# Performance work log

Measured on AMD Instinct MI355X. Metric: run time of the kernel, lower is better.

Reference implementation:

```python
import jax, jax.numpy as jnp
import numpy as np

T, B, D_IN, R, D_OUT = 256, 64, 512, 2048, 128
SPARSITY, BETA, THRESH = 0.8, 0.9, 1.0


def setup_inputs() -> dict:
    key = jax.random.key(0)
    ks = jax.random.split(key, 6)
    lim_rec = float(np.sqrt(3.0 / R))  # VarianceScaling(1.0,'fan_avg','uniform') with fan_in=fan_out=R
    return {
        "x_seq": jax.random.normal(ks[0], (T, B, D_IN), jnp.float32),
        "w_in": jax.random.normal(ks[1], (D_IN, R), jnp.float32) / np.sqrt(D_IN).astype(np.float32),
        "b_in": jnp.zeros((R,), jnp.float32),
        "w_rec": jax.random.uniform(ks[2], (R, R), jnp.float32, -lim_rec, lim_rec),
        "w_head": jax.random.normal(ks[3], (R, D_OUT), jnp.float32) / np.sqrt(R).astype(np.float32),
        "b_head": jnp.zeros((D_OUT,), jnp.float32),
    }


def reference(x_seq, w_in, b_in, w_rec, w_head, b_head):
    n = R * R
    keep = max(1, int(n * (1.0 - SPARSITY)))
    scores = jnp.abs(w_rec).reshape(-1)
    thresh = jnp.sort(scores)[n - keep]  # k-th largest of |w_rec| (same threshold as top_k)
    mask = (jnp.abs(w_rec) >= thresh).astype(w_rec.dtype)
    w_eff = w_rec * mask

    # input projection is time-parallel; hoist it out of the scan
    drive_in = jnp.einsum('tbd,dr->tbr', x_seq, w_in) + b_in  # [T,B,R]

    def step(carry, drive_t):
        V, prev_s = carry
        cur = drive_t + prev_s @ w_eff          # sparse recurrent drive
        V = BETA * V + cur                      # LIF integrate (leak + input)
        s = (V > THRESH).astype(x_seq.dtype)    # heaviside spike
        V = V - s * THRESH                      # soft reset
        logits = s @ w_head + b_head
        return (V, s), (logits, jnp.mean(s))

    init = (jnp.zeros((B, R), x_seq.dtype), jnp.zeros((B, R), x_seq.dtype))
    _, (logits_seq, sr_seq) = jax.lax.scan(step, init, drive_in)

    readout = jnp.mean(logits_seq, axis=0)  # readout mode 'mean'
    spike_rate = jnp.asarray([jnp.mean(sr_seq)])
    active_ratio = jnp.mean(mask)
    return readout, logits_seq, spike_rate, active_ratio
```

## Files before the change

kernel.cpp:

```cpp
#include <hip/hip_runtime.h>
#include <hip/hip_bf16.h>
#include <stdint.h>

#define TT 256
#define BB 64
#define DIN 512
#define RR 2048
#define DOUT 128
#define NTOT (RR*RR)
#define NKEEP 838860
#define BETA 0.9f
#define VTH 1.0f


__global__ void k_init(uint32_t* __restrict__ p, int n) {
    int i = blockIdx.x * blockDim.x + threadIdx.x;
    int stride = gridDim.x * blockDim.x;
    for (; i < n; i += stride) p[i] = 0u;
}

__global__ void k_hist(const float* __restrict__ w_rec, uint32_t* __restrict__ hist,
                       const uint32_t* __restrict__ state, int p) {
    __shared__ uint32_t lh[256];
    lh[threadIdx.x] = 0u;
    __syncthreads();
    uint32_t prefix = (p > 0) ? state[0] : 0u;
    int sh = 24 - 8 * p;
    int i = blockIdx.x * 256 + threadIdx.x;
    int stride = gridDim.x * 256;
    for (; i < NTOT; i += stride) {
        uint32_t u = __float_as_uint(fabsf(w_rec[i]));
        bool ok = (p == 0) || ((u >> (sh + 8)) == prefix);
        if (ok) atomicAdd(&lh[(u >> sh) & 255u], 1u);
    }
    __syncthreads();
    uint32_t v = lh[threadIdx.x];
    if (v) atomicAdd(&hist[threadIdx.x], v);
}

__global__ void k_select(uint32_t* __restrict__ hist, uint32_t* __restrict__ state, int p) {
    __shared__ uint32_t lh[256];
    int tid = threadIdx.x;
    lh[tid] = hist[tid];
    hist[tid] = 0u;
    __syncthreads();
    if (tid == 0) {
        uint32_t remaining = (p == 0) ? (uint32_t)NKEEP : state[1];
        int bin = 255;
        for (; bin > 0; --bin) {
            uint32_t c = lh[bin];
            if (c >= remaining) break;
            remaining -= c;
        }
        uint32_t pref = (p == 0) ? 0u : state[0];
        pref = (pref << 8) | (uint32_t)bin;
        state[0] = pref;
        state[1] = remaining;
        if (p == 3) state[2] = pref;
    }
}

__global__ void k_maskcount(float* __restrict__ w, const uint32_t* __restrict__ state,
                            uint32_t* __restrict__ cnts) {
    uint32_t th = state[2];
    uint32_t c = 0;
    int i = blockIdx.x * blockDim.x + threadIdx.x;
    int stride = gridDim.x * blockDim.x;
    for (; i < NTOT / 4; i += stride) {
        float4 v = *(float4*)&w[i * 4];
        if ((__float_as_uint(v.x) & 0x7fffffffu) >= th) c++; else v.x = 0.0f;
        if ((__float_as_uint(v.y) & 0x7fffffffu) >= th) c++; else v.y = 0.0f;
        if ((__float_as_uint(v.z) & 0x7fffffffu) >= th) c++; else v.z = 0.0f;
        if ((__float_as_uint(v.w) & 0x7fffffffu) >= th) c++; else v.w = 0.0f;
        *(float4*)&w[i * 4] = v;
    }
    for (int off = 32; off > 0; off >>= 1) c += __shfl_down(c, off);
    if ((threadIdx.x & 63) == 0 && c) atomicAdd(&cnts[1], c);
}

__global__ __launch_bounds__(256) void k_drive(const float* __restrict__ x,
                                               const float* __restrict__ w_in,
                                               const float* __restrict__ b_in,
                                               float* __restrict__ drive) {
    __shared__ float As[8][128];
    __shared__ float Bs[8][128];
    const int m0 = blockIdx.x * 128;
    const int n0 = blockIdx.y * 128;
    const int tid = threadIdx.x;
    const int tx = tid & 15, ty = tid >> 4;
    const int ar = tid >> 1;
    const int ak = (tid & 1) * 4;
    const int bk = tid >> 5;
    const int bc = (tid & 31) * 4;
    float acc[8][8];
    #pragma unroll
    for (int i = 0; i < 8; ++i)
        #pragma unroll
        for (int j = 0; j < 8; ++j) acc[i][j] = 0.0f;

    for (int k0 = 0; k0 < DIN; k0 += 8) {
        float4 av = *(const float4*)&x[(m0 + ar) * DIN + k0 + ak];
        float4 bv = *(const float4*)&w_in[(size_t)(k0 + bk) * RR + n0 + bc];
        __syncthreads();
        As[ak + 0][ar] = av.x; As[ak + 1][ar] = av.y;
        As[ak + 2][ar] = av.z; As[ak + 3][ar] = av.w;
        *(float4*)&Bs[bk][bc] = bv;
        __syncthreads();
        #pragma unroll
        for (int kk = 0; kk < 8; ++kk) {
            float a[8], b[8];
            *(float4*)&a[0] = *(const float4*)&As[kk][ty * 8];
            *(float4*)&a[4] = *(const float4*)&As[kk][ty * 8 + 4];
            *(float4*)&b[0] = *(const float4*)&Bs[kk][tx * 8];
            *(float4*)&b[4] = *(const float4*)&Bs[kk][tx * 8 + 4];
            #pragma unroll
            for (int i = 0; i < 8; ++i)
                #pragma unroll
                for (int j = 0; j < 8; ++j)
                    acc[i][j] = fmaf(a[i], b[j], acc[i][j]);
        }
    }
    float bb[8];
    #pragma unroll
    for (int j = 0; j < 8; ++j) bb[j] = b_in[n0 + tx * 8 + j];
    #pragma unroll
    for (int i = 0; i < 8; ++i) {
        size_t row = (size_t)(m0 + ty * 8 + i) * RR + n0 + tx * 8;
        float4 v0, v1;
        v0.x = acc[i][0] + bb[0]; v0.y = acc[i][1] + bb[1];
        v0.z = acc[i][2] + bb[2]; v0.w = acc[i][3] + bb[3];
        v1.x = acc[i][4] + bb[4]; v1.y = acc[i][5] + bb[5];
        v1.z = acc[i][6] + bb[6]; v1.w = acc[i][7] + bb[7];
        *(float4*)&drive[row] = v0;
        *(float4*)&drive[row + 4] = v1;
    }
}

__global__ __launch_bounds__(256) void k_scan(const float* __restrict__ w_rec,
                                              const float* __restrict__ drive,
                                              uint32_t* mask, unsigned long long* flags,
                                              uint32_t* cnts) {
    __shared__ __align__(16) int s_list[RR];
    __shared__ int s_n;
    __shared__ uint32_t s_red[4];

    const int tid = threadIdx.x;
    const int blk = blockIdx.x;
    const int cg = blk & 7;
    const int b = blk >> 3;
    const int col = (cg << 8) + tid;
    const int w = tid >> 6;
    const int lane = tid & 63;
    const char* Wp = (const char*)(w_rec + col);

    float V = 0.f;
    uint32_t scnt = 0;
    float dv = drive[(size_t)b * RR + col];

    for (int t = 0; t < TT; ++t) {
        float a = dv;
        if (t > 0) {
            if (tid == 0) {
                const unsigned long long* fl = &flags[(size_t)(t - 1) * BB + b];
                while (__hip_atomic_load(fl, __ATOMIC_RELAXED, __HIP_MEMORY_SCOPE_AGENT)
                       != ~0ull)
                    __builtin_amdgcn_s_sleep(1);
            }
            __syncthreads();
            if (tid < 64) {
                uint32_t m = __hip_atomic_load(&mask[((size_t)(t - 1) * BB + b) * 64 + tid],
                                               __ATOMIC_RELAXED, __HIP_MEMORY_SCOPE_AGENT);
                int p = __popc(m);
                int off = p;
                #pragma unroll
                for (int d = 1; d < 64; d <<= 1) {
                    int o = __shfl_up(off, d);
                    if (tid >= d) off += o;
                }
                if (tid == 63) s_n = off;
                int e = off - p;
                int base = tid << 5;
                while (m) {
                    int bit = __builtin_ctz(m);
                    m &= m - 1;
                    s_list[e++] = (base + bit) << 13;
                }
            }
            __syncthreads();
            const int n = s_n;
            int i = 0;
            for (; i + 16 <= n; i += 16) {
                int4 o0 = *(const int4*)&s_list[i];
                int4 o1 = *(const int4*)&s_list[i + 4];
                int4 o2 = *(const int4*)&s_list[i + 8];
                int4 o3 = *(const int4*)&s_list[i + 12];
                float v[16];
                v[0]  = *(const float*)(Wp + o0.x);
                v[1]  = *(const float*)(Wp + o0.y);
                v[2]  = *(const float*)(Wp + o0.z);
                v[3]  = *(const float*)(Wp + o0.w);
                v[4]  = *(const float*)(Wp + o1.x);
                v[5]  = *(const float*)(Wp + o1.y);
                v[6]  = *(const float*)(Wp + o1.z);
                v[7]  = *(const float*)(Wp + o1.w);
                v[8]  = *(const float*)(Wp + o2.x);
                v[9]  = *(const float*)(Wp + o2.y);
                v[10] = *(const float*)(Wp + o2.z);
                v[11] = *(const float*)(Wp + o2.w);
                v[12] = *(const float*)(Wp + o3.x);
                v[13] = *(const float*)(Wp + o3.y);
                v[14] = *(const float*)(Wp + o3.z);
                v[15] = *(const float*)(Wp + o3.w);
                #pragma unroll
                for (int j = 0; j < 16; ++j) a += v[j];
            }
            for (; i + 4 <= n; i += 4) {
                int4 o = *(const int4*)&s_list[i];
                float v0 = *(const float*)(Wp + o.x);
                float v1 = *(const float*)(Wp + o.y);
                float v2 = *(const float*)(Wp + o.z);
                float v3 = *(const float*)(Wp + o.w);
                a += v0; a += v1; a += v2; a += v3;
            }
            for (; i < n; ++i) a += *(const float*)(Wp + s_list[i]);
        }

        V = BETA * V + a;
        bool sp = V > VTH;
        if (sp) V -= VTH;

        if (t + 1 < TT)
            dv = drive[((size_t)(t + 1) * BB + b) * RR + col];

        unsigned long long bal = __ballot(sp);
        if (lane == 0) {
            __hip_atomic_store(
                (unsigned long long*)&mask[((size_t)t * BB + b) * 64] + (cg * 4 + w),
                bal, __ATOMIC_RELAXED, __HIP_MEMORY_SCOPE_AGENT);
            scnt += (uint32_t)__popcll(bal);
        }
        __syncthreads();
        if (tid == 0)
            __hip_atomic_store((uint8_t*)&flags[(size_t)t * BB + b] + cg, (uint8_t)0xFF,
                               __ATOMIC_RELEASE, __HIP_MEMORY_SCOPE_AGENT);
    }

    if (lane == 0) s_red[w] = scnt;
    __syncthreads();
    if (tid == 0) {
        uint32_t s = s_red[0] + s_red[1] + s_red[2] + s_red[3];
        if (s) atomicAdd(&cnts[0], s);
    }
}

__global__ __launch_bounds__(128) void k_head(const uint32_t* __restrict__ mask,
                                              const float* __restrict__ w_head,
                                              const float* __restrict__ b_head,
                                              float* __restrict__ logits) {
    __shared__ uint32_t sm[64];
    int tb = blockIdx.x;
    int tid = threadIdx.x;
    if (tid < 64) sm[tid] = mask[tb * 64 + tid];
    __syncthreads();
    float acc = b_head[tid];
    for (int w = 0; w < 64; ++w) {
        uint32_t m = sm[w];
        int base = w << 5;
        while (m) {
            int bit = __builtin_ctz(m);
            m &= m - 1;
            acc += w_head[(size_t)(base + bit) * DOUT + tid];
        }
    }
    logits[(size_t)tb * DOUT + tid] = acc;
}

__global__ __launch_bounds__(128) void k_readout(const float* __restrict__ logits,
                                                 float* __restrict__ readout) {
    int b = blockIdx.x, cidx = threadIdx.x;
    float s = 0.0f;
    for (int t = 0; t < TT; ++t)
        s += logits[(size_t)t * (BB * DOUT) + b * DOUT + cidx];
    readout[b * DOUT + cidx] = s * (1.0f / (float)TT);
}

__global__ void k_scalars(const uint32_t* __restrict__ cnts, float* __restrict__ out) {
    if (threadIdx.x == 0 && blockIdx.x == 0) {
        out[BB * DOUT + TT * BB * DOUT]     = (float)cnts[0] / (float)(TT * BB * RR);
        out[BB * DOUT + TT * BB * DOUT + 1] = (float)cnts[1] / (float)NTOT;
    }
}

extern "C" void kernel_launch(void* const* d_in, const int* in_sizes, int n_in,
                              void* d_out, int out_size, void* d_ws, size_t ws_size,
                              hipStream_t stream) {
    const float* x      = (const float*)d_in[0];
    const float* w_in   = (const float*)d_in[1];
    const float* b_in   = (const float*)d_in[2];
    float*       w_rec  = (float*)d_in[3];
    const float* w_head = (const float*)d_in[4];
    const float* b_head = (const float*)d_in[5];
    float* out = (float*)d_out;

    float*    drive = (float*)d_ws;
    uint32_t* mask  = (uint32_t*)((char*)d_ws + 134217728u);
    unsigned long long* flags = (unsigned long long*)(mask + (TT * BB * 64));
    uint32_t* hist  = (uint32_t*)(flags + TT * BB);
    uint32_t* state = hist + 256;
    uint32_t* cnts  = state + 8;

    k_init<<<64, 256, 0, stream>>>((uint32_t*)flags, TT * BB * 2 + 256 + 8 + 2);

    for (int p = 0; p < 4; ++p) {
        k_hist<<<1024, 256, 0, stream>>>(w_rec, hist, state, p);
        k_select<<<1, 256, 0, stream>>>(hist, state, p);
    }
    k_maskcount<<<1024, 256, 0, stream>>>(w_rec, state, cnts);

    k_drive<<<dim3(128, 16), 256, 0, stream>>>(x, w_in, b_in, drive);

    k_scan<<<512, 256, 0, stream>>>(w_rec, drive, mask, flags, cnts);

    k_head<<<TT * BB, 128, 0, stream>>>(mask, w_head, b_head, out + BB * DOUT);
    k_readout<<<BB, 128, 0, stream>>>(out + BB * DOUT, out);
    k_scalars<<<1, 64, 0, stream>>>(cnts, out);
}
```

Measured before the change: 5.007 ms.

## Swizzle masked recurrent weights and decouple scan wavefronts with per-wave flags

The masking kernel now also XOR-swizzles 64-column groups inside each row of the recurrent weight matrix, so each scan wavefront reads its columns from a row-dependent rotated location. This is meant to spread the gather traffic across memory channels. The scan kernel drops its block-wide barriers. Each wavefront waits on a 32-bit flag, builds its own spike list and publishes its ballot with an atomic fetch-or, which removes intra-block synchronisation from the recurrent loop. The cost is four times the shared-memory lists, more atomics on the flags, and a swizzle kernel launched with 2048 blocks of 1024 threads.

```diff
diff --git a/kernel.cpp b/kernel.cpp
--- a/kernel.cpp
+++ b/kernel.cpp
@@ -60,22 +60,36 @@
     }
 }
 
-__global__ void k_maskcount(float* __restrict__ w, const uint32_t* __restrict__ state,
-                            uint32_t* __restrict__ cnts) {
-    uint32_t th = state[2];
+__global__ __launch_bounds__(1024) void k_swz(float* __restrict__ w,
+                                              const uint32_t* __restrict__ state,
+                                              uint32_t* __restrict__ cnts) {
+    const int r = blockIdx.x;
+    const uint32_t th = state[2];
+    const int m = r & 31;
+    const int tid = threadIdx.x;
     uint32_t c = 0;
-    int i = blockIdx.x * blockDim.x + threadIdx.x;
-    int stride = gridDim.x * blockDim.x;
-    for (; i < NTOT / 4; i += stride) {
-        float4 v = *(float4*)&w[i * 4];
-        if ((__float_as_uint(v.x) & 0x7fffffffu) >= th) c++; else v.x = 0.0f;
-        if ((__float_as_uint(v.y) & 0x7fffffffu) >= th) c++; else v.y = 0.0f;
-        if ((__float_as_uint(v.z) & 0x7fffffffu) >= th) c++; else v.z = 0.0f;
-        if ((__float_as_uint(v.w) & 0x7fffffffu) >= th) c++; else v.w = 0.0f;
-        *(float4*)&w[i * 4] = v;
+    if (m == 0) {
+        for (int k = tid; k < RR; k += 1024) {
+            float v = w[(size_t)r * RR + k];
+            if ((__float_as_uint(v) & 0x7fffffffu) >= th) c++;
+            else w[(size_t)r * RR + k] = 0.0f;
+        }
+    } else {
+        const int h = 31 - __clz(m);
+        const int p = tid >> 6;
+        const int lane = tid & 63;
+        const int g = ((p >> h) << (h + 1)) | (p & ((1 << h) - 1));
+        const int g2 = g ^ m;
+        const size_t i1 = (size_t)r * RR + (g << 6) + lane;
+        const size_t i2 = (size_t)r * RR + (g2 << 6) + lane;
+        float v1 = w[i1], v2 = w[i2];
+        if ((__float_as_uint(v1) & 0x7fffffffu) >= th) c++; else v1 = 0.0f;
+        if ((__float_as_uint(v2) & 0x7fffffffu) >= th) c++; else v2 = 0.0f;
+        w[i1] = v2;
+        w[i2] = v1;
     }
     for (int off = 32; off > 0; off >>= 1) c += __shfl_down(c, off);
-    if ((threadIdx.x & 63) == 0 && c) atomicAdd(&cnts[1], c);
+    if ((tid & 63) == 0 && c) atomicAdd(&cnts[1], c);
 }
 
 __global__ __launch_bounds__(256) void k_drive(const float* __restrict__ x,
@@ -136,22 +150,23 @@
     }
 }
 
-__global__ __launch_bounds__(256) void k_scan(const float* __restrict__ w_rec,
-                                              const float* __restrict__ drive,
-                                              uint32_t* mask, unsigned long long* flags,
-                                              uint32_t* cnts) {
-    __shared__ __align__(16) int s_list[RR];
-    __shared__ int s_n;
-    __shared__ uint32_t s_red[4];
+__global__ __launch_bounds__(256, 2) void k_scan(const float* __restrict__ w_rec,
+                                                 const float* __restrict__ drive,
+                                                 unsigned long long* mask,
+                                                 uint32_t* flags, uint32_t* cnts) {
+    __shared__ __align__(16) int s_list[4 * RR];
 
     const int tid = threadIdx.x;
     const int blk = blockIdx.x;
     const int cg = blk & 7;
     const int b = blk >> 3;
-    const int col = (cg << 8) + tid;
     const int w = tid >> 6;
     const int lane = tid & 63;
-    const char* Wp = (const char*)(w_rec + col);
+    const int g = cg * 4 + w;
+    const int col = (g << 6) + lane;
+    int* wl = &s_list[w << 11];
+    const char* Wp = (const char*)w_rec + (lane << 2);
+    const uint32_t fbit = 1u << g;
 
     float V = 0.f;
     uint32_t scnt = 0;
@@ -160,69 +175,62 @@
     for (int t = 0; t < TT; ++t) {
         float a = dv;
         if (t > 0) {
-            if (tid == 0) {
-                const unsigned long long* fl = &flags[(size_t)(t - 1) * BB + b];
-                while (__hip_atomic_load(fl, __ATOMIC_RELAXED, __HIP_MEMORY_SCOPE_AGENT)
-                       != ~0ull)
-                    __builtin_amdgcn_s_sleep(1);
+            const uint32_t* fl = &flags[(t - 1) * BB + b];
+            while (__hip_atomic_load(fl, __ATOMIC_RELAXED, __HIP_MEMORY_SCOPE_AGENT)
+                   != 0xFFFFFFFFu)
+                __builtin_amdgcn_s_sleep(1);
+            asm volatile("" ::: "memory");
+            uint32_t m = __hip_atomic_load(
+                (const uint32_t*)(mask + (size_t)((t - 1) * BB + b) * 32) + lane,
+                __ATOMIC_RELAXED, __HIP_MEMORY_SCOPE_AGENT);
+            int p = __popc(m);
+            int off = p;
+            #pragma unroll
+            for (int d = 1; d < 64; d <<= 1) {
+                int o = __shfl_up(off, d);
+                if (lane >= d) off += o;
             }
-            __syncthreads();
-            if (tid < 64) {
-                uint32_t m = __hip_atomic_load(&mask[((size_t)(t - 1) * BB + b) * 64 + tid],
-                                               __ATOMIC_RELAXED, __HIP_MEMORY_SCOPE_AGENT);
-                int p = __popc(m);
-                int off = p;
+            const int n = __shfl(off, 63);
+            int e = off - p;
+            int base = lane << 5;
+            while (m) {
+                int bit = __builtin_ctz(m);
+                m &= m - 1;
+                int row = base + bit;
+                wl[e++] = (row << 13) | ((((row & 31) ^ g)) << 8);
+            }
+            __threadfence_block();
+            int i = 0;
+            for (; i + 32 <= n; i += 32) {
+                int4 o[8];
                 #pragma unroll
-                for (int d = 1; d < 64; d <<= 1) {
-                    int o = __shfl_up(off, d);
-                    if (tid >= d) off += o;
+                for (int j = 0; j < 8; ++j) o[j] = *(const int4*)&wl[i + 4 * j];
+                float v[32];
+                #pragma unroll
+                for (int j = 0; j < 8; ++j) {
+                    v[4 * j + 0] = *(const float*)(Wp + o[j].x);
+                    v[4 * j + 1] = *(const float*)(Wp + o[j].y);
+                    v[4 * j + 2] = *(const float*)(Wp + o[j].z);
+                    v[4 * j + 3] = *(const float*)(Wp + o[j].w);
                 }
-                if (tid == 63) s_n = off;
-                int e = off - p;
-                int base = tid << 5;
-                while (m) {
-                    int bit = __builtin_ctz(m);
-                    m &= m - 1;
-                    s_list[e++] = (base + bit) << 13;
-                }
+                #pragma unroll
+                for (int j = 0; j < 32; ++j) a += v[j];
             }
-            __syncthreads();
-            const int n = s_n;
-            int i = 0;
-            for (; i + 16 <= n; i += 16) {
-                int4 o0 = *(const int4*)&s_list[i];
-                int4 o1 = *(const int4*)&s_list[i + 4];
-                int4 o2 = *(const int4*)&s_list[i + 8];
-                int4 o3 = *(const int4*)&s_list[i + 12];
-                float v[16];
-                v[0]  = *(const float*)(Wp + o0.x);
-                v[1]  = *(const float*)(Wp + o0.y);
-                v[2]  = *(const float*)(Wp + o0.z);
-                v[3]  = *(const float*)(Wp + o0.w);
-                v[4]  = *(const float*)(Wp + o1.x);
-                v[5]  = *(const float*)(Wp + o1.y);
-                v[6]  = *(const float*)(Wp + o1.z);
-                v[7]  = *(const float*)(Wp + o1.w);
-                v[8]  = *(const float*)(Wp + o2.x);
-                v[9]  = *(const float*)(Wp + o2.y);
-                v[10] = *(const float*)(Wp + o2.z);
-                v[11] = *(const float*)(Wp + o2.w);
-                v[12] = *(const float*)(Wp + o3.x);
-                v[13] = *(const float*)(Wp + o3.y);
-                v[14] = *(const float*)(Wp + o3.z);
-                v[15] = *(const float*)(Wp + o3.w);
-                #pragma unroll
-                for (int j = 0; j < 16; ++j) a += v[j];
+            for (; i + 8 <= n; i += 8) {
+                int4 o0 = *(const int4*)&wl[i];
+                int4 o1 = *(const int4*)&wl[i + 4];
+                float v0 = *(const float*)(Wp + o0.x);
+                float v1 = *(const float*)(Wp + o0.y);
+                float v2 = *(const float*)(Wp + o0.z);
+                float v3 = *(const float*)(Wp + o0.w);
+                float v4 = *(const float*)(Wp + o1.x);
+                float v5 = *(const float*)(Wp + o1.y);
+                float v6 = *(const float*)(Wp + o1.z);
+                float v7 = *(const float*)(Wp + o1.w);
+                a += v0; a += v1; a += v2; a += v3;
+                a += v4; a += v5; a += v6; a += v7;
             }
-            for (; i + 4 <= n; i += 4) {
-                int4 o = *(const int4*)&s_list[i];
-                float v0 = *(const float*)(Wp + o.x);
-                float v1 = *(const float*)(Wp + o.y);
-                float v2 = *(const float*)(Wp + o.z);
-                float v3 = *(const float*)(Wp + o.w);
-                a += v0; a += v1; a += v2; a += v3;
-            }
-            for (; i < n; ++i) a += *(const float*)(Wp + s_list[i]);
+            for (; i < n; ++i) a += *(const float*)(Wp + wl[i]);
         }
 
         V = BETA * V + a;
@@ -230,27 +238,19 @@
         if (sp) V -= VTH;
 
         if (t + 1 < TT)
-            dv = drive[((size_t)(t + 1) * BB + b) * RR + col];
+            dv = drive[(size_t)(t + 1) * (BB * RR) + (size_t)b * RR + col];
 
         unsigned long long bal = __ballot(sp);
         if (lane == 0) {
-            __hip_atomic_store(
-                (unsigned long long*)&mask[((size_t)t * BB + b) * 64] + (cg * 4 + w),
-                bal, __ATOMIC_RELAXED, __HIP_MEMORY_SCOPE_AGENT);
+            __hip_atomic_store(mask + (size_t)(t * BB + b) * 32 + g, bal,
+                               __ATOMIC_RELAXED, __HIP_MEMORY_SCOPE_AGENT);
             scnt += (uint32_t)__popcll(bal);
-        }
-        __syncthreads();
-        if (tid == 0)
-            __hip_atomic_store((uint8_t*)&flags[(size_t)t * BB + b] + cg, (uint8_t)0xFF,
-                               __ATOMIC_RELEASE, __HIP_MEMORY_SCOPE_AGENT);
-    }
-
-    if (lane == 0) s_red[w] = scnt;
-    __syncthreads();
-    if (tid == 0) {
-        uint32_t s = s_red[0] + s_red[1] + s_red[2] + s_red[3];
-        if (s) atomicAdd(&cnts[0], s);
-    }
+            (void)__hip_atomic_fetch_or(&flags[t * BB + b], fbit,
+                                        __ATOMIC_RELEASE, __HIP_MEMORY_SCOPE_AGENT);
+        }
+    }
+
+    if (lane == 0 && scnt) atomicAdd(&cnts[0], scnt);
 }
 
 __global__ __launch_bounds__(128) void k_head(const uint32_t* __restrict__ mask,
@@ -303,25 +303,26 @@
     float* out = (float*)d_out;
 
     float*    drive = (float*)d_ws;
-    uint32_t* mask  = (uint32_t*)((char*)d_ws + 134217728u);
-    unsigned long long* flags = (unsigned long long*)(mask + (TT * BB * 64));
-    uint32_t* hist  = (uint32_t*)(flags + TT * BB);
+    unsigned long long* mask = (unsigned long long*)((char*)d_ws + 134217728u);
+    uint32_t* flags = (uint32_t*)(mask + (size_t)TT * BB * 32);
+    uint32_t* hist  = flags + TT * BB;
     uint32_t* state = hist + 256;
     uint32_t* cnts  = state + 8;
 
-    k_init<<<64, 256, 0, stream>>>((uint32_t*)flags, TT * BB * 2 + 256 + 8 + 2);
+    k_init<<<64, 256, 0, stream>>>(flags, TT * BB + 256 + 8 + 2);
 
     for (int p = 0; p < 4; ++p) {
         k_hist<<<1024, 256, 0, stream>>>(w_rec, hist, state, p);
         k_select<<<1, 256, 0, stream>>>(hist, state, p);
     }
-    k_maskcount<<<1024, 256, 0, stream>>>(w_rec, state, cnts);
+    k_swz<<<RR, 1024, 0, stream>>>(w_rec, state, cnts);
 
     k_drive<<<dim3(128, 16), 256, 0, stream>>>(x, w_in, b_in, drive);
 
     k_scan<<<512, 256, 0, stream>>>(w_rec, drive, mask, flags, cnts);
 
-    k_head<<<TT * BB, 128, 0, stream>>>(mask, w_head, b_head, out + BB * DOUT);
+    k_head<<<TT * BB, 128, 0, stream>>>((const uint32_t*)mask, w_head, b_head,
+                                        out + BB * DOUT);
     k_readout<<<BB, 128, 0, stream>>>(out + BB * DOUT, out);
     k_scalars<<<1, 64, 0, stream>>>(cnts, out);
 }
```

Measured after the change: 14.84 ms. +196.4%, slower.

## Swizzle recurrent weight columns per row to spread gather accesses across channels

Applied to the files above, without the earlier changes.

Replaces the mask kernel with one that masks w_rec and also XOR-swizzles 64-column groups within each 256-column block based on row index mod 4. The scan's gather addresses apply the matching XOR, so the four wavefronts of a block touch different group offsets for the same spiking row, which should reduce channel/bank aliasing at the 8KB row stride. The gather loop is also unrolled to 32 loads, and the scan gets a launch-bounds occupancy hint. It adds layout complexity and more register pressure.

```diff
diff --git a/kernel.cpp b/kernel.cpp
--- a/kernel.cpp
+++ b/kernel.cpp
@@ -60,22 +60,39 @@
     }
 }
 
-__global__ void k_maskcount(float* __restrict__ w, const uint32_t* __restrict__ state,
-                            uint32_t* __restrict__ cnts) {
-    uint32_t th = state[2];
+__global__ __launch_bounds__(1024) void k_swz(float* __restrict__ w,
+                                              const uint32_t* __restrict__ state,
+                                              uint32_t* __restrict__ cnts) {
+    const int r = blockIdx.x;
+    const uint32_t th = state[2];
+    const int m = r & 3;
+    const int tid = threadIdx.x;
     uint32_t c = 0;
-    int i = blockIdx.x * blockDim.x + threadIdx.x;
-    int stride = gridDim.x * blockDim.x;
-    for (; i < NTOT / 4; i += stride) {
-        float4 v = *(float4*)&w[i * 4];
-        if ((__float_as_uint(v.x) & 0x7fffffffu) >= th) c++; else v.x = 0.0f;
-        if ((__float_as_uint(v.y) & 0x7fffffffu) >= th) c++; else v.y = 0.0f;
-        if ((__float_as_uint(v.z) & 0x7fffffffu) >= th) c++; else v.z = 0.0f;
-        if ((__float_as_uint(v.w) & 0x7fffffffu) >= th) c++; else v.w = 0.0f;
-        *(float4*)&w[i * 4] = v;
+    if (m == 0) {
+        #pragma unroll
+        for (int q = 0; q < 2; ++q) {
+            size_t i = (size_t)r * RR + q * 1024 + tid;
+            float v = w[i];
+            if ((__float_as_uint(v) & 0x7fffffffu) >= th) c++;
+            else w[i] = 0.0f;
+        }
+    } else {
+        const int h = (m == 1) ? 0 : 1;
+        const int chunk = tid >> 7;
+        const int pair = (tid >> 6) & 1;
+        const int lane = tid & 63;
+        const int g  = (h == 0) ? (pair << 1) : pair;
+        const int g2 = g ^ m;
+        const size_t i1 = (size_t)r * RR + chunk * 256 + g  * 64 + lane;
+        const size_t i2 = (size_t)r * RR + chunk * 256 + g2 * 64 + lane;
+        float v1 = w[i1], v2 = w[i2];
+        if ((__float_as_uint(v1) & 0x7fffffffu) >= th) c++; else v1 = 0.0f;
+        if ((__float_as_uint(v2) & 0x7fffffffu) >= th) c++; else v2 = 0.0f;
+        w[i1] = v2;
+        w[i2] = v1;
     }
     for (int off = 32; off > 0; off >>= 1) c += __shfl_down(c, off);
-    if ((threadIdx.x & 63) == 0 && c) atomicAdd(&cnts[1], c);
+    if ((tid & 63) == 0 && c) atomicAdd(&cnts[1], c);
 }
 
 __global__ __launch_bounds__(256) void k_drive(const float* __restrict__ x,
@@ -136,10 +153,10 @@
     }
 }
 
-__global__ __launch_bounds__(256) void k_scan(const float* __restrict__ w_rec,
-                                              const float* __restrict__ drive,
-                                              uint32_t* mask, unsigned long long* flags,
-                                              uint32_t* cnts) {
+__global__ __launch_bounds__(256, 2) void k_scan(const float* __restrict__ w_rec,
+                                                 const float* __restrict__ drive,
+                                                 uint32_t* mask, unsigned long long* flags,
+                                                 uint32_t* cnts) {
     __shared__ __align__(16) int s_list[RR];
     __shared__ int s_n;
     __shared__ uint32_t s_red[4];
@@ -148,10 +165,11 @@
     const int blk = blockIdx.x;
     const int cg = blk & 7;
     const int b = blk >> 3;
-    const int col = (cg << 8) + tid;
     const int w = tid >> 6;
     const int lane = tid & 63;
-    const char* Wp = (const char*)(w_rec + col);
+    const int col = (cg << 8) + tid;
+    const int wx = w << 8;
+    const char* Wq = (const char*)w_rec + (cg << 10) + (lane << 2);
 
     float V = 0.f;
     uint32_t scnt = 0;
@@ -183,46 +201,43 @@
                 while (m) {
                     int bit = __builtin_ctz(m);
                     m &= m - 1;
-                    s_list[e++] = (base + bit) << 13;
+                    int row = base + bit;
+                    s_list[e++] = (row << 13) | ((row & 3) << 8);
                 }
             }
             __syncthreads();
             const int n = s_n;
             int i = 0;
-            for (; i + 16 <= n; i += 16) {
+            for (; i + 32 <= n; i += 32) {
+                int4 o[8];
+                #pragma unroll
+                for (int j = 0; j < 8; ++j) o[j] = *(const int4*)&s_list[i + 4 * j];
+                float v[32];
+                #pragma unroll
+                for (int j = 0; j < 8; ++j) {
+                    v[4 * j + 0] = *(const float*)(Wq + (o[j].x ^ wx));
+                    v[4 * j + 1] = *(const float*)(Wq + (o[j].y ^ wx));
+                    v[4 * j + 2] = *(const float*)(Wq + (o[j].z ^ wx));
+                    v[4 * j + 3] = *(const float*)(Wq + (o[j].w ^ wx));
+                }
+                #pragma unroll
+                for (int j = 0; j < 32; ++j) a += v[j];
+            }
+            for (; i + 8 <= n; i += 8) {
                 int4 o0 = *(const int4*)&s_list[i];
                 int4 o1 = *(const int4*)&s_list[i + 4];
-                int4 o2 = *(const int4*)&s_list[i + 8];
-                int4 o3 = *(const int4*)&s_list[i + 12];
-                float v[16];
-                v[0]  = *(const float*)(Wp + o0.x);
-                v[1]  = *(const float*)(Wp + o0.y);
-                v[2]  = *(const float*)(Wp + o0.z);
-                v[3]  = *(const float*)(Wp + o0.w);
-                v[4]  = *(const float*)(Wp + o1.x);
-                v[5]  = *(const float*)(Wp + o1.y);
-                v[6]  = *(const float*)(Wp + o1.z);
-                v[7]  = *(const float*)(Wp + o1.w);
-                v[8]  = *(const float*)(Wp + o2.x);
-                v[9]  = *(const float*)(Wp + o2.y);
-                v[10] = *(const float*)(Wp + o2.z);
-                v[11] = *(const float*)(Wp + o2.w);
-                v[12] = *(const float*)(Wp + o3.x);
-                v[13] = *(const float*)(Wp + o3.y);
-                v[14] = *(const float*)(Wp + o3.z);
-                v[15] = *(const float*)(Wp + o3.w);
-                #pragma unroll
-                for (int j = 0; j < 16; ++j) a += v[j];
+                float v0 = *(const float*)(Wq + (o0.x ^ wx));
+                float v1 = *(const float*)(Wq + (o0.y ^ wx));
+                float v2 = *(const float*)(Wq + (o0.z ^ wx));
+                float v3 = *(const float*)(Wq + (o0.w ^ wx));
+                float v4 = *(const float*)(Wq + (o1.x ^ wx));
+                float v5 = *(const float*)(Wq + (o1.y ^ wx));
+                float v6 = *(const float*)(Wq + (o1.z ^ wx));
+                float v7 = *(const float*)(Wq + (o1.w ^ wx));
+                a += v0; a += v1; a += v2; a += v3;
+                a += v4; a += v5; a += v6; a += v7;
             }
-            for (; i + 4 <= n; i += 4) {
-                int4 o = *(const int4*)&s_list[i];
-                float v0 = *(const float*)(Wp + o.x);
-                float v1 = *(const float*)(Wp + o.y);
-                float v2 = *(const float*)(Wp + o.z);
-                float v3 = *(const float*)(Wp + o.w);
-                a += v0; a += v1; a += v2; a += v3;
-            }
-            for (; i < n; ++i) a += *(const float*)(Wp + s_list[i]);
+            for (; i < n; ++i) a += *(const float*)(Wq + (s_list[i] ^ wx));
         }
 
         V = BETA * V + a;
@@ -315,7 +330,7 @@
         k_hist<<<1024, 256, 0, stream>>>(w_rec, hist, state, p);
         k_select<<<1, 256, 0, stream>>>(hist, state, p);
     }
-    k_maskcount<<<1024, 256, 0, stream>>>(w_rec, state, cnts);
+    k_swz<<<RR, 1024, 0, stream>>>(w_rec, state, cnts);
 
     k_drive<<<dim3(128, 16), 256, 0, stream>>>(x, w_in, b_in, drive);
 
```

After: 5.425 ms. 8.4% more time.
